# Kernel optimization log

Measured on AMD Instinct MI355X. Metric: run time of the kernel, lower is better.

Reference implementation:

```python
import jax, jax.numpy as jnp
import numpy as np


def setup_inputs() -> dict:
    key = jax.random.key(0)
    k1, k2, k3, k4 = jax.random.split(key, 4)
    B, NEG, S = 16, 128, 128
    D_PRED, D_SAMP, N_PRED = 512, 512, 12
    c = jax.random.normal(k1, (B, S, D_PRED), dtype=jnp.float32)
    z = jax.random.normal(k2, (B, NEG, S, D_SAMP), dtype=jnp.float32)
    # stacked nn.Linear params: W[i] is [out=dimSample, in=dimPrediction]
    W = jax.random.normal(k3, (N_PRED, D_SAMP, D_PRED), dtype=jnp.float32) / np.sqrt(D_PRED)
    b = jax.random.normal(k4, (N_PRED, D_SAMP), dtype=jnp.float32) * 0.01
    return {"c": c, "z": z, "W": W, "b": b, "k": 3}


def reference(c, z, W, b, k):
    # select the k-th predictor Linear: c_proj = c @ W[k]^T + b[k]  -> [B, S, dimSample]
    c_proj = jnp.einsum("bsd,od->bso", c, W[k]) + b[k]
    # (c_proj[:, None] * z).mean(dim=3) expressed as a batched dot product -> [B, Neg, S]
    d_samp = z.shape[-1]
    out = jnp.einsum("bso,bnso->bns", c_proj, z) / d_samp
    return out
```

## Files before the change

### kernel.cpp

```cpp
#include <hip/hip_runtime.h>

#define DIM 512
#define M_ROWS 2048

typedef __attribute__((ext_vector_type(8))) short short8;
typedef __attribute__((ext_vector_type(4))) float f32x4;

static __device__ __forceinline__ short f2bf(float x) {
    unsigned int u = __builtin_bit_cast(unsigned int, x);
    u += 0x7fffu + ((u >> 16) & 1u);
    return (short)(u >> 16);
}

#define K1_PAD 40
__global__ __launch_bounds__(256) void cproj_mfma(
    const float* __restrict__ c, const float* __restrict__ W,
    const float* __restrict__ bias, const int* __restrict__ kptr,
    float* __restrict__ cp) {
    const int ksel = kptr[0];
    const float* __restrict__ Wk = W + (size_t)ksel * DIM * DIM;
    const float* __restrict__ bk = bias + (size_t)ksel * DIM;

    __shared__ short Alds[64][K1_PAD];
    __shared__ short Blds[64][K1_PAD];

    const int bm = blockIdx.x & 31;
    const int bn = blockIdx.x >> 5;
    const int t  = threadIdx.x;
    const int lane = t & 63;
    const int wv   = t >> 6;

    const int srow = t >> 2;
    const int sk   = (t & 3) * 8;

    const float* Ap = c  + (size_t)(bm * 64 + srow) * DIM + sk;
    const float* Bp = Wk + (size_t)(bn * 64 + srow) * DIM + sk;

    float4 a0 = *(const float4*)Ap,       a1 = *(const float4*)(Ap + 4);
    float4 b0 = *(const float4*)Bp,       b1 = *(const float4*)(Bp + 4);

    f32x4 acc[4] = {};

    const int frow = lane & 15;
    const int fk   = (lane >> 4) * 8;

    for (int step = 0; step < 16; ++step) {
        __syncthreads();
        short8 av, bv;
        av[0] = f2bf(a0.x); av[1] = f2bf(a0.y); av[2] = f2bf(a0.z); av[3] = f2bf(a0.w);
        av[4] = f2bf(a1.x); av[5] = f2bf(a1.y); av[6] = f2bf(a1.z); av[7] = f2bf(a1.w);
        bv[0] = f2bf(b0.x); bv[1] = f2bf(b0.y); bv[2] = f2bf(b0.z); bv[3] = f2bf(b0.w);
        bv[4] = f2bf(b1.x); bv[5] = f2bf(b1.y); bv[6] = f2bf(b1.z); bv[7] = f2bf(b1.w);
        *(short8*)&Alds[srow][sk] = av;
        *(short8*)&Blds[srow][sk] = bv;
        __syncthreads();
        if (step < 15) {
            const int off = (step + 1) * 32;
            a0 = *(const float4*)(Ap + off); a1 = *(const float4*)(Ap + off + 4);
            b0 = *(const float4*)(Bp + off); b1 = *(const float4*)(Bp + off + 4);
        }
        const short8 bfrag = *(const short8*)&Blds[wv * 16 + frow][fk];
#pragma unroll
        for (int f = 0; f < 4; ++f) {
            const short8 afrag = *(const short8*)&Alds[f * 16 + frow][fk];
            acc[f] = __builtin_amdgcn_mfma_f32_16x16x32_bf16(afrag, bfrag, acc[f], 0, 0, 0);
        }
    }

    const int col = bn * 64 + wv * 16 + frow;
    const float bias_v = bk[col];
    const int r0 = (lane >> 4) * 4;
#pragma unroll
    for (int f = 0; f < 4; ++f)
#pragma unroll
        for (int r = 0; r < 4; ++r)
            cp[(size_t)(bm * 64 + f * 16 + r0 + r) * DIM + col] = acc[f][r] + bias_v;
}

#define NSTR ((size_t)4 * 128 * 512)
#define HALF 256
#define LD4(p) (*(const float4*)(p))

__global__ __launch_bounds__(256, 6) void dot_kernel(
    const float* __restrict__ z, const float* __restrict__ cp,
    float* __restrict__ out) {
    const int bs   = blockIdx.x;
    const int wave = threadIdx.x >> 6;
    const int lane = threadIdx.x & 63;
    const int b = bs >> 7;
    const int s = bs & 127;

    const float* cpr = cp + (size_t)bs * DIM + lane * 4;
    const float4 c0 = LD4(cpr);
    const float4 c1 = LD4(cpr + HALF);

    const float* zp = z + (((size_t)(b * 128 + wave)) * 128 + s) * DIM + lane * 4;
    float* outp = out + ((size_t)b * 128 + wave) * 128 + s;

    float4 zA0 = LD4(zp + 0 * NSTR), zA1 = LD4(zp + 0 * NSTR + HALF);
    float4 zB0 = LD4(zp + 1 * NSTR), zB1 = LD4(zp + 1 * NSTR + HALF);
    float4 zC0 = LD4(zp + 2 * NSTR), zC1 = LD4(zp + 2 * NSTR + HALF);
    float4 zD0 = LD4(zp + 3 * NSTR), zD1 = LD4(zp + 3 * NSTR + HALF);

#define SLOT(Z0, Z1, II)                                                      \
    {                                                                          \
        float acc = Z0.x * c0.x;                                               \
        acc = fmaf(Z0.y, c0.y, acc);                                           \
        acc = fmaf(Z0.z, c0.z, acc);                                           \
        acc = fmaf(Z0.w, c0.w, acc);                                           \
        acc = fmaf(Z1.x, c1.x, acc);                                           \
        acc = fmaf(Z1.y, c1.y, acc);                                           \
        acc = fmaf(Z1.z, c1.z, acc);                                           \
        acc = fmaf(Z1.w, c1.w, acc);                                           \
        if ((II) + 4 < 32) {             \
            Z0 = LD4(zp + (size_t)((II) + 4) * NSTR);                          \
            Z1 = LD4(zp + (size_t)((II) + 4) * NSTR + HALF);                   \
        }                                                                      \
        _Pragma("unroll")                                                      \
        for (int off = 32; off; off >>= 1) acc += __shfl_xor(acc, off);        \
        if (lane == 0) outp[(size_t)(II) * 4 * 128] = acc * (1.0f / 512.0f);   \
    }

#pragma unroll
    for (int g = 0; g < 8; ++g) {
        SLOT(zA0, zA1, g * 4 + 0)
        SLOT(zB0, zB1, g * 4 + 1)
        SLOT(zC0, zC1, g * 4 + 2)
        SLOT(zD0, zD1, g * 4 + 3)
    }
#undef SLOT
}

extern "C" void kernel_launch(void* const* d_in, const int* in_sizes, int n_in,
                              void* d_out, int out_size, void* d_ws, size_t ws_size,
                              hipStream_t stream) {
    const float* c    = (const float*)d_in[0];
    const float* z    = (const float*)d_in[1];
    const float* W    = (const float*)d_in[2];
    const float* bias = (const float*)d_in[3];
    const int*   kptr = (const int*)d_in[4];
    float* out = (float*)d_out;
    float* cp  = (float*)d_ws;

    cproj_mfma<<<dim3(256), dim3(256), 0, stream>>>(c, W, bias, kptr, cp);
    dot_kernel<<<dim3(2048), dim3(256), 0, stream>>>(z, cp, out);
}
```

Before: 119.0 us.

## Stream z through LDS with async global_load_lds double buffering

The dot kernel now loads z through global_load_lds 16-byte transfers into a per-wave, double-buffered LDS area instead of holding the rows in registers. Each wave stages the next group of four negatives while it reduces the current group, and explicit vmcnt waits handle ordering. The aim is to keep more memory traffic in flight and cut register pressure in this bandwidth-bound streaming loop. The 64KB of LDS per block, with the occupancy hint of 6 removed, limits how many blocks fit on each CU, which can reduce latency hiding.

```diff
diff --git a/kernel.cpp b/kernel.cpp
--- a/kernel.cpp
+++ b/kernel.cpp
@@ -78,12 +78,20 @@
 }
 
 #define NSTR ((size_t)4 * 128 * 512)
-#define HALF 256
-#define LD4(p) (*(const float4*)(p))
 
-__global__ __launch_bounds__(256, 6) void dot_kernel(
+typedef const __attribute__((address_space(1))) void* gas_ptr;
+typedef __attribute__((address_space(3))) void* las_ptr;
+
+static __device__ __forceinline__ void stage1k(const float* g, float* l) {
+    __builtin_amdgcn_global_load_lds((gas_ptr)(const void*)g, (las_ptr)(void*)l,
+                                     16, 0, 0);
+}
+
+__global__ __launch_bounds__(256) void dot_kernel_lds(
     const float* __restrict__ z, const float* __restrict__ cp,
     float* __restrict__ out) {
+    __shared__ float buf[4][2][4][512];
+
     const int bs   = blockIdx.x;
     const int wave = threadIdx.x >> 6;
     const int lane = threadIdx.x & 63;
@@ -91,44 +99,52 @@
     const int s = bs & 127;
 
     const float* cpr = cp + (size_t)bs * DIM + lane * 4;
-    const float4 c0 = LD4(cpr);
-    const float4 c1 = LD4(cpr + HALF);
+    const float4 c0 = *(const float4*)cpr;
+    const float4 c1 = *(const float4*)(cpr + 256);
 
     const float* zp = z + (((size_t)(b * 128 + wave)) * 128 + s) * DIM + lane * 4;
     float* outp = out + ((size_t)b * 128 + wave) * 128 + s;
 
-    float4 zA0 = LD4(zp + 0 * NSTR), zA1 = LD4(zp + 0 * NSTR + HALF);
-    float4 zB0 = LD4(zp + 1 * NSTR), zB1 = LD4(zp + 1 * NSTR + HALF);
-    float4 zC0 = LD4(zp + 2 * NSTR), zC1 = LD4(zp + 2 * NSTR + HALF);
-    float4 zD0 = LD4(zp + 3 * NSTR), zD1 = LD4(zp + 3 * NSTR + HALF);
-
-#define SLOT(Z0, Z1, II)                                                      \
+#define STAGE_GROUP(GG, BSEL)                                                  \
     {                                                                          \
-        float acc = Z0.x * c0.x;                                               \
-        acc = fmaf(Z0.y, c0.y, acc);                                           \
-        acc = fmaf(Z0.z, c0.z, acc);                                           \
-        acc = fmaf(Z0.w, c0.w, acc);                                           \
-        acc = fmaf(Z1.x, c1.x, acc);                                           \
-        acc = fmaf(Z1.y, c1.y, acc);                                           \
-        acc = fmaf(Z1.z, c1.z, acc);                                           \
-        acc = fmaf(Z1.w, c1.w, acc);                                           \
-        if ((II) + 4 < 32) {             \
-            Z0 = LD4(zp + (size_t)((II) + 4) * NSTR);                          \
-            Z1 = LD4(zp + (size_t)((II) + 4) * NSTR + HALF);                   \
+        _Pragma("unroll")                                                      \
+        for (int sl = 0; sl < 4; ++sl) {                                       \
+            const float* gsrc = zp + (size_t)((GG) * 4 + sl) * NSTR;           \
+            stage1k(gsrc,       &buf[wave][BSEL][sl][0]);                      \
+            stage1k(gsrc + 256, &buf[wave][BSEL][sl][256]);                    \
         }                                                                      \
-        _Pragma("unroll")                                                      \
-        for (int off = 32; off; off >>= 1) acc += __shfl_xor(acc, off);        \
-        if (lane == 0) outp[(size_t)(II) * 4 * 128] = acc * (1.0f / 512.0f);   \
     }
 
+    STAGE_GROUP(0, 0)
+
+    for (int g = 0; g < 8; ++g) {
+        if (g < 7) {
+            STAGE_GROUP(g + 1, (g + 1) & 1)
+            asm volatile("s_waitcnt vmcnt(8)" ::: "memory");
+        } else {
+            asm volatile("s_waitcnt vmcnt(0)" ::: "memory");
+        }
+        __builtin_amdgcn_sched_barrier(0);
+        const int bsel = g & 1;
 #pragma unroll
-    for (int g = 0; g < 8; ++g) {
-        SLOT(zA0, zA1, g * 4 + 0)
-        SLOT(zB0, zB1, g * 4 + 1)
-        SLOT(zC0, zC1, g * 4 + 2)
-        SLOT(zD0, zD1, g * 4 + 3)
+        for (int sl = 0; sl < 4; ++sl) {
+            const float4 z0 = *(const float4*)&buf[wave][bsel][sl][lane * 4];
+            const float4 z1 = *(const float4*)&buf[wave][bsel][sl][256 + lane * 4];
+            float acc = z0.x * c0.x;
+            acc = fmaf(z0.y, c0.y, acc);
+            acc = fmaf(z0.z, c0.z, acc);
+            acc = fmaf(z0.w, c0.w, acc);
+            acc = fmaf(z1.x, c1.x, acc);
+            acc = fmaf(z1.y, c1.y, acc);
+            acc = fmaf(z1.z, c1.z, acc);
+            acc = fmaf(z1.w, c1.w, acc);
+#pragma unroll
+            for (int off = 32; off; off >>= 1) acc += __shfl_xor(acc, off);
+            if (lane == 0)
+                outp[(size_t)(g * 4 + sl) * 4 * 128] = acc * (1.0f / 512.0f);
+        }
     }
-#undef SLOT
+#undef STAGE_GROUP
 }
 
 extern "C" void kernel_launch(void* const* d_in, const int* in_sizes, int n_in,
@@ -143,5 +159,5 @@
     float* cp  = (float*)d_ws;
 
     cproj_mfma<<<dim3(256), dim3(256), 0, stream>>>(c, W, bias, kptr, cp);
-    dot_kernel<<<dim3(2048), dim3(256), 0, stream>>>(z, cp, out);
+    dot_kernel_lds<<<dim3(2048), dim3(256), 0, stream>>>(z, cp, out);
 }
```

Measured after the change: 116.3 us. 1.02x faster.
